# Performance work log

Hardware: AMD Instinct MI355X
Metric: run time of the kernel (lower is better)

## Reference

```python
import jax, jax.numpy as jnp
import numpy as np
from jax import lax

C = 512          # in_channels
L = 4            # fcos_conv_layers
NUM_CLS = 1      # fcos_num_class - 1
PRIOR_BIAS = float(-np.log((1 - 0.01) / 0.01))
BN_EPS = 1e-5


def conv1d(x, w, b, pad):
    # x: [B, Cin, T], w: [Cout, Cin, K]
    y = lax.conv_general_dilated(x, w, window_strides=(1,), padding=[(pad, pad)],
                                 dimension_numbers=('NCH', 'OIH', 'NCH'))
    return y + b[None, :, None]


def bn(x, g, b, m, v):
    inv = lax.rsqrt(v + BN_EPS)
    return (x - m[None, :, None]) * (g * inv)[None, :, None] + b[None, :, None]


def tower(x, ws, bs, gs, bes, ms, vs):
    # ws: [L, C, C, 3]; fixed small loop over layers
    for i in range(L):
        x = jax.nn.relu(bn(conv1d(x, ws[i], bs[i], 1), gs[i], bes[i], ms[i], vs[i]))
    return x


def setup_inputs() -> dict:
    key = jax.random.key(0)
    ks = jax.random.split(key, 32)
    d = {}
    d['f0'] = jax.random.normal(ks[0], (8, C, 1024), jnp.float32)
    d['f1'] = jax.random.normal(ks[1], (8, C, 512), jnp.float32)
    d['f2'] = jax.random.normal(ks[2], (8, C, 256), jnp.float32)

    def nrm(k, shape):
        return 0.01 * jax.random.normal(k, shape, jnp.float32)

    # cls / bbox towers: stacked conv + BN params
    d['cls_tw_w'] = nrm(ks[3], (L, C, C, 3)); d['cls_tw_b'] = jnp.zeros((L, C))
    d['cls_bn_g'] = jnp.ones((L, C)); d['cls_bn_b'] = jnp.zeros((L, C))
    d['cls_bn_m'] = jnp.zeros((L, C)); d['cls_bn_v'] = jnp.ones((L, C))
    d['box_tw_w'] = nrm(ks[4], (L, C, C, 3)); d['box_tw_b'] = jnp.zeros((L, C))
    d['box_bn_g'] = jnp.ones((L, C)); d['box_bn_b'] = jnp.zeros((L, C))
    d['box_bn_m'] = jnp.zeros((L, C)); d['box_bn_v'] = jnp.ones((L, C))

    d['logits_w'] = nrm(ks[5], (NUM_CLS, C, 3))
    d['logits_b'] = jnp.full((NUM_CLS,), PRIOR_BIAS, jnp.float32)
    d['bbox_w'] = nrm(ks[6], (2, C, 3)); d['bbox_b'] = jnp.zeros((2,))

    d['mix_w'] = nrm(ks[7], (C, 2 * C, 1)); d['mix_b'] = jnp.zeros((C,))
    d['mix_bn_g'] = jnp.ones((C,)); d['mix_bn_b'] = jnp.zeros((C,))
    d['mix_bn_m'] = jnp.zeros((C,)); d['mix_bn_v'] = jnp.ones((C,))

    d['iou_w1'] = nrm(ks[8], (C // 2, C, 3)); d['iou_b1'] = jnp.zeros((C // 2,))
    d['iou_bn_g'] = jnp.ones((C // 2,)); d['iou_bn_b'] = jnp.zeros((C // 2,))
    d['iou_bn_m'] = jnp.zeros((C // 2,)); d['iou_bn_v'] = jnp.ones((C // 2,))
    d['iou_w2'] = nrm(ks[9], (1, C // 2, 1)); d['iou_b2'] = jnp.zeros((1,))

    d['scales'] = jnp.ones((3,), jnp.float32)
    return d


def reference(f0, f1, f2,
              cls_tw_w, cls_tw_b, cls_bn_g, cls_bn_b, cls_bn_m, cls_bn_v,
              box_tw_w, box_tw_b, box_bn_g, box_bn_b, box_bn_m, box_bn_v,
              logits_w, logits_b, bbox_w, bbox_b,
              mix_w, mix_b, mix_bn_g, mix_bn_b, mix_bn_m, mix_bn_v,
              iou_w1, iou_b1, iou_bn_g, iou_bn_b, iou_bn_m, iou_bn_v,
              iou_w2, iou_b2, scales):
    outs = []
    for l, x in enumerate([f0, f1, f2]):
        ct = tower(x, cls_tw_w, cls_tw_b, cls_bn_g, cls_bn_b, cls_bn_m, cls_bn_v)
        bt = tower(x, box_tw_w, box_tw_b, box_bn_g, box_bn_b, box_bn_m, box_bn_v)
        logits = conv1d(ct, logits_w, logits_b, 1)                      # [B, 1, T]
        bbox = jnp.exp(conv1d(bt, bbox_w, bbox_b, 1) * scales[l])       # [B, 2, T]
        mix = jax.nn.relu(bn(conv1d(jnp.concatenate([ct, bt], axis=1), mix_w, mix_b, 0),
                             mix_bn_g, mix_bn_b, mix_bn_m, mix_bn_v))   # [B, C, T]
        h = jax.nn.relu(bn(conv1d(mix, iou_w1, iou_b1, 1),
                           iou_bn_g, iou_bn_b, iou_bn_m, iou_bn_v))
        iou = conv1d(h, iou_w2, iou_b2, 0)                              # [B, 1, T]
        outs.append(jnp.concatenate([logits, bbox, iou], axis=1))       # [B, 4, T]
    return jnp.concatenate(outs, axis=-1)  # [B, 4, T0+T1+T2]
```

## Files before the change

kernel.cpp:

```cpp
#include <hip/hip_runtime.h>
#include <hip/hip_bf16.h>


typedef __bf16 bf16x8 __attribute__((ext_vector_type(8)));
typedef float f32x4 __attribute__((ext_vector_type(4)));

__device__ __forceinline__ float bf2f(unsigned short u) {
    union { unsigned int i; float f; } c; c.i = ((unsigned int)u) << 16; return c.f;
}
__device__ __forceinline__ unsigned short f2bf(float f) {
    union { __hip_bfloat16 h; unsigned short u; } c; c.h = __float2bfloat16(f); return c.u;
}

__device__ __forceinline__ void gload16(const void* g, void* l) {
    __builtin_amdgcn_global_load_lds(
        (const __attribute__((address_space(1))) unsigned int*)g,
        (__attribute__((address_space(3))) unsigned int*)l,
        16, 0, 0);
}

__global__ __launch_bounds__(512, 2)
void conv_tower(const unsigned short* __restrict__ X, int xstride, int ci_twstride,
                const unsigned short* __restrict__ W,
                const float* __restrict__ Bs,
                unsigned short* __restrict__ Y)
{
    constexpr int XHALF = 17 * 512;
    constexpr int WHALF = 48 * 512;
    __shared__ alignas(16) unsigned short Xs[2 * XHALF];
    __shared__ alignas(16) unsigned short Wsh[2 * WHALF];

    const int L = blockIdx.x;
    const int P = (L & 7) * 28 + (L >> 3);
    const int tt = P >> 2, sub = P & 3;
    const int tw = sub >> 1, co0 = (sub & 1) << 8;

    int rowstart;
    if (tt < 32)      { rowstart = (tt >> 2) * 1026 + 1 + ((tt & 3) << 8); }
    else if (tt < 48) { int i = tt - 32; rowstart = 8208 + (i >> 1) * 514 + 1 + ((i & 1) << 8); }
    else              { rowstart = 12320 + (tt - 48) * 258 + 1; }

    const int tid = threadIdx.x;
    const int lane = tid & 63, wid = tid >> 6;
    const int wco = (wid >> 2) << 7;
    const int wt  = (wid & 3) << 6;
    const int lr = lane & 15;
    const int sr = lane >> 4;

    const unsigned short* Wp = W + (size_t)tw * 3145728;
    const float* Bp = Bs + tw * 2048;
    const int co_out0 = tw * 512 + co0;
    const int ci_off = tw * ci_twstride;

    const unsigned short* xga[3]; unsigned short* xl0[3];
#pragma unroll
    for (int p = 0; p < 3; ++p) {
        int seg = (p < 2) ? (p * 8 + wid) : 16;
        xl0[p] = Xs + seg * 512;
        int g = seg * 64 + lane;
        int row = g >> 2, sc = (g & 3) ^ ((row >> 1) & 3);
        xga[p] = X + (size_t)(rowstart - 1 + row) * xstride + ci_off + sc * 8;
    }
    const unsigned short* wga[6]; unsigned short* wl0[6];
#pragma unroll
    for (int p = 0; p < 6; ++p) {
        int seg = p * 8 + wid;
        wl0[p] = Wsh + seg * 512;
        int g = seg * 64 + lane;
        int row = g >> 2, sc = (g & 3) ^ ((row >> 1) & 3);
        int co = row & 255, kk = row >> 8;
        wga[p] = Wp + (size_t)(co0 + co) * 1536 + kk * 512 + sc * 8;
    }

    f32x4 acc[8][4];
#pragma unroll
    for (int i = 0; i < 8; ++i)
#pragma unroll
        for (int j = 0; j < 4; ++j) acc[i][j] = (f32x4){0.f, 0.f, 0.f, 0.f};

#pragma unroll
    for (int p = 0; p < 3; ++p) { gload16(xga[p], xl0[p]); xga[p] += 32; }
#pragma unroll
    for (int p = 0; p < 6; ++p) { gload16(wga[p], wl0[p]); wga[p] += 32; }
    asm volatile("s_waitcnt vmcnt(0)" ::: "memory");
    __builtin_amdgcn_s_barrier();

    int cur = 0;
    for (int ks = 0; ks < 16; ++ks) {
        const bool notlast = (ks < 15);
        const char* bX = (const char*)Xs + cur * (XHALF * 2);
        const char* bW = (const char*)Wsh + cur * (WHALF * 2);
#pragma unroll
        for (int kk = 0; kk < 3; ++kk) {
            bf16x8 af[8], bv[4];
#pragma unroll
            for (int mi = 0; mi < 8; ++mi) {
                int ra = kk * 256 + wco + mi * 16 + lr;
                af[mi] = *(const bf16x8*)(bW + ra * 64 + (((sr ^ (ra >> 1)) & 3) << 4));
            }
#pragma unroll
            for (int ni = 0; ni < 4; ++ni) {
                int rb = wt + ni * 16 + lr + kk;
                bv[ni] = *(const bf16x8*)(bX + rb * 64 + (((sr ^ (rb >> 1)) & 3) << 4));
            }
            if (notlast) {
                if (kk == 0) {
#pragma unroll
                    for (int p = 0; p < 3; ++p) { gload16(xga[p], xl0[p] + (cur ^ 1) * XHALF); xga[p] += 32; }
                } else {
#pragma unroll
                    for (int p = 0; p < 3; ++p) {
                        int q = (kk - 1) * 3 + p;
                        gload16(wga[q], wl0[q] + (cur ^ 1) * WHALF); wga[q] += 32;
                    }
                }
            }
            __builtin_amdgcn_s_barrier();
            asm volatile("s_waitcnt lgkmcnt(0)" ::: "memory");
            __builtin_amdgcn_sched_barrier(0);
            __builtin_amdgcn_s_setprio(1);
#pragma unroll
            for (int mi = 0; mi < 8; ++mi)
#pragma unroll
                for (int ni = 0; ni < 4; ++ni)
                    acc[mi][ni] = __builtin_amdgcn_mfma_f32_16x16x32_bf16(af[mi], bv[ni], acc[mi][ni], 0, 0, 0);
            __builtin_amdgcn_s_setprio(0);
        }
        if (notlast) asm volatile("s_waitcnt vmcnt(0)" ::: "memory");
        __builtin_amdgcn_s_barrier();
        cur ^= 1;
    }

    const int r4 = sr * 4;
#pragma unroll
    for (int mi = 0; mi < 8; ++mi) {
        int co_l = wco + mi * 16 + r4;
        float b0 = Bp[co0 + co_l + 0], b1 = Bp[co0 + co_l + 1];
        float b2 = Bp[co0 + co_l + 2], b3 = Bp[co0 + co_l + 3];
#pragma unroll
        for (int ni = 0; ni < 4; ++ni) {
            int t = wt + ni * 16 + lr;
            f32x4 a = acc[mi][ni];
            float v0 = fmaxf(a[0] + b0, 0.f), v1 = fmaxf(a[1] + b1, 0.f);
            float v2 = fmaxf(a[2] + b2, 0.f), v3 = fmaxf(a[3] + b3, 0.f);
            union { unsigned long long u; unsigned short s[4]; } pk;
            pk.s[0] = f2bf(v0); pk.s[1] = f2bf(v1); pk.s[2] = f2bf(v2); pk.s[3] = f2bf(v3);
            *(unsigned long long*)(Y + (size_t)(rowstart + t) * 1024 + co_out0 + co_l) = pk.u;
        }
    }
}

__device__ __forceinline__ void tile_decode(int ct, int& rowstart, int& t0, int& Tl) {
    if (ct < 64)      { Tl = 1024; int b = ct >> 3;                 t0 = (ct & 7) << 7; rowstart = b * 1026 + 1; }
    else if (ct < 96) { Tl = 512;  int i = ct - 64; int b = i >> 2; t0 = (i & 3) << 7; rowstart = 8208 + b * 514 + 1; }
    else              { Tl = 256;  int i = ct - 96; int b = i >> 1; t0 = (i & 1) << 7; rowstart = 12320 + b * 258 + 1; }
}

template<int KSIZE>
__global__ __launch_bounds__(256)
void conv_gemm(const unsigned short* __restrict__ X, int xstride, int ci0_base, int ci_twstride, int Cin,
               const unsigned short* __restrict__ W, int w_twstride,
               const float* __restrict__ Bs, int b_twstride,
               unsigned short* __restrict__ Y, int ystride, int co_twstride,
               int relu)
{
    constexpr int BM = 128, BN = 128, BK = 32;
    constexpr int NR = BN + KSIZE - 1;
    constexpr int XSEG = (NR * 64 + 1023) / 1024;
    constexpr int XPW  = (XSEG + 3) / 4;
    constexpr int WSEG = KSIZE * BM * 64 / 1024;
    constexpr int WPW  = WSEG / 4;
    __shared__ alignas(16) unsigned short Xs[2 * XSEG * 512];
    __shared__ alignas(16) unsigned short Ws[2 * WSEG * 512];

    const int tid = threadIdx.x;
    const int lane = tid & 63, wid = tid >> 6;
    int rowstart, t0, Tl;
    tile_decode(blockIdx.x, rowstart, t0, Tl);
    const int co0 = blockIdx.y * BM;
    const int tw = blockIdx.z;
    const int ci_off = ci0_base + tw * ci_twstride;
    const unsigned short* Wp = W + (size_t)tw * w_twstride;
    const float* Bp = Bs + tw * b_twstride;
    const int co_out0 = tw * co_twstride + co0;

    const int wm = (wid >> 1) * 64, wn = (wid & 1) * 64;
    const int lr = lane & 15;
    const int sr = lane >> 4;

    const unsigned short* xga[XPW]; unsigned short* xl[XPW];
#pragma unroll
    for (int p = 0; p < XPW; ++p) {
        int seg = (KSIZE == 3) ? ((p < 2) ? p * 4 + wid : 8) : (p * 4 + wid);
        xl[p] = Xs + seg * 512;
        int g = seg * 64 + lane;
        int row = g >> 2, s = (g & 3) ^ ((row >> 1) & 3);
        xga[p] = X + (size_t)(rowstart - (KSIZE >> 1) + row) * xstride + ci_off + s * 8;
    }
    const unsigned short* wga[WPW]; unsigned short* wl[WPW];
#pragma unroll
    for (int p = 0; p < WPW; ++p) {
        int seg = p * 4 + wid;
        wl[p] = Ws + seg * 512;
        int g = seg * 64 + lane;
        int row = g >> 2, s = (g & 3) ^ ((row >> 1) & 3);
        int co = row & (BM - 1), kk = row >> 7;
        wga[p] = Wp + (size_t)(co0 + co) * (KSIZE * Cin) + kk * Cin + s * 8;
    }

    f32x4 acc[4][4];
#pragma unroll
    for (int i = 0; i < 4; ++i)
#pragma unroll
        for (int j = 0; j < 4; ++j) acc[i][j] = (f32x4){0.f, 0.f, 0.f, 0.f};

    auto STAGE = [&](int buf) {
#pragma unroll
        for (int p = 0; p < XPW; ++p) { gload16(xga[p], xl[p] + buf * (XSEG * 512)); xga[p] += BK; }
#pragma unroll
        for (int p = 0; p < WPW; ++p) { gload16(wga[p], wl[p] + buf * (WSEG * 512)); wga[p] += BK; }
    };

    const int nk = Cin / BK;
    STAGE(0);
    int cur = 0;
    for (int ks = 0; ks < nk; ++ks) {
        if (ks + 1 < nk) {
            STAGE(cur ^ 1);
            if constexpr (KSIZE == 3) asm volatile("s_waitcnt vmcnt(9)" ::: "memory");
            else                      asm volatile("s_waitcnt vmcnt(4)" ::: "memory");
        } else {
            asm volatile("s_waitcnt vmcnt(0)" ::: "memory");
        }
        __builtin_amdgcn_sched_barrier(0);
        __builtin_amdgcn_s_barrier();

        const char* bXs = (const char*)Xs + cur * (XSEG * 1024);
        const char* bWs = (const char*)Ws + cur * (WSEG * 1024);
#pragma unroll
        for (int kk = 0; kk < KSIZE; ++kk) {
            bf16x8 af[4], bv[4];
#pragma unroll
            for (int mi = 0; mi < 4; ++mi) {
                int ra = kk * BM + wm + mi * 16 + lr;
                af[mi] = *(const bf16x8*)(bWs + ra * 64 + (((sr ^ (ra >> 1)) & 3) << 4));
                int rb = wn + mi * 16 + lr + kk;
                bv[mi] = *(const bf16x8*)(bXs + rb * 64 + (((sr ^ (rb >> 1)) & 3) << 4));
            }
#pragma unroll
            for (int mi = 0; mi < 4; ++mi)
#pragma unroll
                for (int ni = 0; ni < 4; ++ni)
                    acc[mi][ni] = __builtin_amdgcn_mfma_f32_16x16x32_bf16(af[mi], bv[ni], acc[mi][ni], 0, 0, 0);
        }
        __builtin_amdgcn_sched_barrier(0);
        __builtin_amdgcn_s_barrier();
        cur ^= 1;
    }

    const int r4 = (lane >> 4) * 4;
#pragma unroll
    for (int mi = 0; mi < 4; ++mi) {
        int co_l = wm + mi * 16 + r4;
        float b0 = Bp[co0 + co_l + 0], b1 = Bp[co0 + co_l + 1];
        float b2 = Bp[co0 + co_l + 2], b3 = Bp[co0 + co_l + 3];
#pragma unroll
        for (int ni = 0; ni < 4; ++ni) {
            int t = t0 + wn + ni * 16 + lr;
            f32x4 a = acc[mi][ni];
            float v0 = a[0] + b0, v1 = a[1] + b1, v2 = a[2] + b2, v3 = a[3] + b3;
            if (relu) {
                v0 = fmaxf(v0, 0.f); v1 = fmaxf(v1, 0.f);
                v2 = fmaxf(v2, 0.f); v3 = fmaxf(v3, 0.f);
            }
            union { unsigned long long u; unsigned short s[4]; } pk;
            pk.s[0] = f2bf(v0); pk.s[1] = f2bf(v1); pk.s[2] = f2bf(v2); pk.s[3] = f2bf(v3);
            *(unsigned long long*)(Y + (size_t)(rowstart + t) * ystride + co_out0 + co_l) = pk.u;
        }
    }
}

__global__ __launch_bounds__(256)
void zero_pads(unsigned short* __restrict__ act0, unsigned short* __restrict__ catA,
               unsigned short* __restrict__ catB, unsigned short* __restrict__ mixo,
               unsigned short* __restrict__ iouh)
{
    int c = blockIdx.x >> 1, side = blockIdx.x & 1;
    int start, Tl;
    if (c < 8)       { start = c * 1026;               Tl = 1024; }
    else if (c < 16) { start = 8208 + (c - 8) * 514;   Tl = 512;  }
    else             { start = 12320 + (c - 16) * 258; Tl = 256;  }
    size_t prow = start + (side ? Tl + 1 : 0);
    int tid = threadIdx.x;
    uint4 z = make_uint4(0u, 0u, 0u, 0u);
    if (tid < 64)  *(uint4*)(act0 + prow * 512 + tid * 8) = z;
    if (tid < 128) { *(uint4*)(catA + prow * 1024 + tid * 8) = z;
                     *(uint4*)(catB + prow * 1024 + tid * 8) = z; }
    if (tid >= 128 && tid < 192) *(uint4*)(mixo + prow * 512 + (tid - 128) * 8) = z;
    if (tid >= 192 && tid < 224) *(uint4*)(iouh + prow * 256 + (tid - 192) * 8) = z;
}

__global__ __launch_bounds__(256)
void transpose_in(const float* __restrict__ f0, const float* __restrict__ f1, const float* __restrict__ f2,
                  unsigned short* __restrict__ act0)
{
    __shared__ float tile[32][33];
    int bx = blockIdx.x;
    const float* src; int Tl, padbase, b, t0;
    if (bx < 256)      { src = f0; Tl = 1024; int i = bx;       b = i >> 5; t0 = (i & 31) << 5; padbase = b * 1026; }
    else if (bx < 384) { src = f1; Tl = 512;  int i = bx - 256; b = i >> 4; t0 = (i & 15) << 5; padbase = 8208 + b * 514; }
    else               { src = f2; Tl = 256;  int i = bx - 384; b = i >> 3; t0 = (i & 7)  << 5; padbase = 12320 + b * 258; }
    int c0 = blockIdx.y << 5;
    const float* sb = src + (size_t)b * 512 * Tl;
    int tl = threadIdx.x & 31, cl = threadIdx.x >> 5;
#pragma unroll
    for (int j = 0; j < 4; ++j) {
        int c = cl + j * 8;
        tile[c][tl] = sb[(size_t)(c0 + c) * Tl + t0 + tl];
    }
    __syncthreads();
    int cc = threadIdx.x & 31, tr0 = threadIdx.x >> 5;
    size_t base = (size_t)(padbase + 1 + t0) * 512 + c0;
#pragma unroll
    for (int j = 0; j < 4; ++j) {
        int tr = tr0 + j * 8;
        act0[base + (size_t)tr * 512 + cc] = f2bf(tile[cc][tr]);
    }
}

__global__ __launch_bounds__(256)
void prep_tower(const float* __restrict__ cls_w, const float* __restrict__ box_w,
                const float* __restrict__ cg, const float* __restrict__ cvv,
                const float* __restrict__ bg, const float* __restrict__ bvv,
                unsigned short* __restrict__ Wt)
{
    int idx = blockIdx.x * 256 + threadIdx.x;
    if (idx >= 2 * 4 * 512 * 3 * 512) return;
    int ci = idx & 511;
    int kk = (idx >> 9) % 3;
    int co = (idx / 1536) & 511;
    int l  = (idx / 786432) & 3;
    int tw = idx / 3145728;
    const float* w = tw ? box_w : cls_w;
    const float* g = tw ? bg : cg;
    const float* v = tw ? bvv : cvv;
    float s = g[l * 512 + co] * rsqrtf(v[l * 512 + co] + 1e-5f);
    float val = w[(((size_t)(l * 512 + co)) * 512 + ci) * 3 + kk] * s;
    Wt[idx] = f2bf(val);
}

__global__ __launch_bounds__(256)
void prep_misc(const float* mix_w, const float* mix_b, const float* mg, const float* mbeta, const float* mm, const float* mv,
               const float* iou_w1, const float* iou_b1, const float* ig, const float* ibeta, const float* im, const float* iv,
               const float* cls_b, const float* cg, const float* cbeta, const float* cm, const float* cv2,
               const float* box_b, const float* bg, const float* bbeta, const float* bm, const float* bv2,
               unsigned short* Wmix, unsigned short* Wiou, float* Bt, float* Bmix, float* Biou)
{
    int idx = blockIdx.x * 256 + threadIdx.x;
    if (idx < 524288) {
        int co = idx >> 10;
        float s = mg[co] * rsqrtf(mv[co] + 1e-5f);
        Wmix[idx] = f2bf(mix_w[idx] * s);
        return;
    }
    idx -= 524288;
    if (idx < 393216) {
        int ci = idx & 511, kk = (idx >> 9) % 3, co = idx / 1536;
        float s = ig[co] * rsqrtf(iv[co] + 1e-5f);
        Wiou[idx] = f2bf(iou_w1[((size_t)(co * 512 + ci)) * 3 + kk] * s);
        return;
    }
    idx -= 393216;
    if (idx < 4096) {
        int co = idx & 511, l = (idx >> 9) & 3, tw = idx >> 11;
        const float* g = tw ? bg : cg; const float* v = tw ? bv2 : cv2;
        const float* m = tw ? bm : cm; const float* be = tw ? bbeta : cbeta;
        const float* cb = tw ? box_b : cls_b;
        int o = l * 512 + co;
        float s = g[o] * rsqrtf(v[o] + 1e-5f);
        Bt[idx] = (cb[o] - m[o]) * s + be[o];
        return;
    }
    idx -= 4096;
    if (idx < 512) {
        float s = mg[idx] * rsqrtf(mv[idx] + 1e-5f);
        Bmix[idx] = (mix_b[idx] - mm[idx]) * s + mbeta[idx];
        return;
    }
    idx -= 512;
    if (idx < 256) {
        float s = ig[idx] * rsqrtf(iv[idx] + 1e-5f);
        Biou[idx] = (iou_b1[idx] - im[idx]) * s + ibeta[idx];
    }
}

__global__ __launch_bounds__(256)
void heads_kernel(const unsigned short* __restrict__ catb, const unsigned short* __restrict__ iouh,
                  const float* __restrict__ lw, const float* __restrict__ lb,
                  const float* __restrict__ bw, const float* __restrict__ bb,
                  const float* __restrict__ iw, const float* __restrict__ ib,
                  const float* __restrict__ scales, float* __restrict__ out)
{
    const int lane = threadIdx.x & 63;
    const int wid = threadIdx.x >> 6;

    float lwr[24], bwr0[24], bwr1[24], iwr[4];
    {
        const float4* p = (const float4*)(lw + lane * 24);
#pragma unroll
        for (int q = 0; q < 6; ++q) {
            float4 v = p[q];
            lwr[q * 4 + 0] = v.x; lwr[q * 4 + 1] = v.y; lwr[q * 4 + 2] = v.z; lwr[q * 4 + 3] = v.w;
        }
        p = (const float4*)(bw + lane * 24);
#pragma unroll
        for (int q = 0; q < 6; ++q) {
            float4 v = p[q];
            bwr0[q * 4 + 0] = v.x; bwr0[q * 4 + 1] = v.y; bwr0[q * 4 + 2] = v.z; bwr0[q * 4 + 3] = v.w;
        }
        p = (const float4*)(bw + 1536 + lane * 24);
#pragma unroll
        for (int q = 0; q < 6; ++q) {
            float4 v = p[q];
            bwr1[q * 4 + 0] = v.x; bwr1[q * 4 + 1] = v.y; bwr1[q * 4 + 2] = v.z; bwr1[q * 4 + 3] = v.w;
        }
        float4 v = *(const float4*)(iw + lane * 4);
        iwr[0] = v.x; iwr[1] = v.y; iwr[2] = v.z; iwr[3] = v.w;
    }
    const float lb0 = lb[0], bb0 = bb[0], bb1 = bb[1], ib0 = ib[0];
    const float s0 = scales[0], s1 = scales[1], s2 = scales[2];

    for (int r = blockIdx.x * 4 + wid; r < 14336; r += gridDim.x * 4) {
        int tlog, roff, tgoff, padbase; float sc;
        if (r < 8192)       { tlog = 10; roff = 0;     tgoff = 0;    sc = s0; }
        else if (r < 12288) { tlog = 9;  roff = 8192;  tgoff = 1024; sc = s1; }
        else                { tlog = 8;  roff = 12288; tgoff = 1536; sc = s2; }
        int i = r - roff;
        int Tl = 1 << tlog;
        int b = i >> tlog, t = i & (Tl - 1);
        if (r < 8192)       padbase = b * 1026;
        else if (r < 12288) padbase = 8208 + b * 514;
        else                padbase = 12320 + b * 258;
        int prow = padbase + 1 + t;

        float al = 0.f, a0 = 0.f, a1 = 0.f, ai = 0.f;
        const unsigned short* base = catb + (size_t)prow * 1024 + lane * 8;
#pragma unroll
        for (int kk = 0; kk < 3; ++kk) {
            union { uint4 u; unsigned short s[8]; } cv, bv;
            cv.u = *(const uint4*)(base + (kk - 1) * 1024);
            bv.u = *(const uint4*)(base + (kk - 1) * 1024 + 512);
#pragma unroll
            for (int j = 0; j < 8; ++j) {
                float xc = bf2f(cv.s[j]);
                float xb = bf2f(bv.s[j]);
                al = fmaf(xc, lwr[j * 3 + kk], al);
                a0 = fmaf(xb, bwr0[j * 3 + kk], a0);
                a1 = fmaf(xb, bwr1[j * 3 + kk], a1);
            }
        }
        {
            union { uint2 u; unsigned short s[4]; } hv;
            hv.u = *(const uint2*)(iouh + (size_t)prow * 256 + lane * 4);
#pragma unroll
            for (int j = 0; j < 4; ++j) ai = fmaf(bf2f(hv.s[j]), iwr[j], ai);
        }
#pragma unroll
        for (int off = 32; off > 0; off >>= 1) {
            al += __shfl_xor(al, off);
            a0 += __shfl_xor(a0, off);
            a1 += __shfl_xor(a1, off);
            ai += __shfl_xor(ai, off);
        }
        if (lane == 0) {
            int tg = tgoff + t;
            out[((size_t)b * 4 + 0) * 1792 + tg] = al + lb0;
            out[((size_t)b * 4 + 1) * 1792 + tg] = expf((a0 + bb0) * sc);
            out[((size_t)b * 4 + 2) * 1792 + tg] = expf((a1 + bb1) * sc);
            out[((size_t)b * 4 + 3) * 1792 + tg] = ai + ib0;
        }
    }
}

extern "C" void kernel_launch(void* const* d_in, const int* in_sizes, int n_in,
                              void* d_out, int out_size, void* d_ws, size_t ws_size,
                              hipStream_t stream)
{
    const float* f0       = (const float*)d_in[0];
    const float* f1       = (const float*)d_in[1];
    const float* f2       = (const float*)d_in[2];
    const float* cls_tw_w = (const float*)d_in[3];
    const float* cls_tw_b = (const float*)d_in[4];
    const float* cls_bn_g = (const float*)d_in[5];
    const float* cls_bn_b = (const float*)d_in[6];
    const float* cls_bn_m = (const float*)d_in[7];
    const float* cls_bn_v = (const float*)d_in[8];
    const float* box_tw_w = (const float*)d_in[9];
    const float* box_tw_b = (const float*)d_in[10];
    const float* box_bn_g = (const float*)d_in[11];
    const float* box_bn_b = (const float*)d_in[12];
    const float* box_bn_m = (const float*)d_in[13];
    const float* box_bn_v = (const float*)d_in[14];
    const float* logits_w = (const float*)d_in[15];
    const float* logits_b = (const float*)d_in[16];
    const float* bbox_w   = (const float*)d_in[17];
    const float* bbox_b   = (const float*)d_in[18];
    const float* mix_w    = (const float*)d_in[19];
    const float* mix_b    = (const float*)d_in[20];
    const float* mix_bn_g = (const float*)d_in[21];
    const float* mix_bn_b = (const float*)d_in[22];
    const float* mix_bn_m = (const float*)d_in[23];
    const float* mix_bn_v = (const float*)d_in[24];
    const float* iou_w1   = (const float*)d_in[25];
    const float* iou_b1   = (const float*)d_in[26];
    const float* iou_bn_g = (const float*)d_in[27];
    const float* iou_bn_b = (const float*)d_in[28];
    const float* iou_bn_m = (const float*)d_in[29];
    const float* iou_bn_v = (const float*)d_in[30];
    const float* iou_w2   = (const float*)d_in[31];
    const float* iou_b2   = (const float*)d_in[32];
    const float* scales   = (const float*)d_in[33];

    unsigned char* ws = (unsigned char*)d_ws;
    unsigned short* Wt   = (unsigned short*)(ws + 0);
    unsigned short* Wmix = (unsigned short*)(ws + 12582912);
    unsigned short* Wiou = (unsigned short*)(ws + 13631488);
    float*          Bt   = (float*)(ws + 14417920);
    float*          Bmix = (float*)(ws + 14434304);
    float*          Biou = (float*)(ws + 14436352);
    unsigned short* act0 = (unsigned short*)(ws + 14437376);
    unsigned short* catA = (unsigned short*)(ws + 29182976);
    unsigned short* catB = (unsigned short*)(ws + 58674176);
    unsigned short* mixo = (unsigned short*)(ws + 88165376);
    unsigned short* iouh = (unsigned short*)(ws + 102910976);

    zero_pads<<<dim3(48), dim3(256), 0, stream>>>(act0, catA, catB, mixo, iouh);
    prep_tower<<<dim3(24576), dim3(256), 0, stream>>>(cls_tw_w, box_tw_w, cls_bn_g, cls_bn_v,
                                                      box_bn_g, box_bn_v, Wt);
    prep_misc<<<dim3(3603), dim3(256), 0, stream>>>(mix_w, mix_b, mix_bn_g, mix_bn_b, mix_bn_m, mix_bn_v,
                                                    iou_w1, iou_b1, iou_bn_g, iou_bn_b, iou_bn_m, iou_bn_v,
                                                    cls_tw_b, cls_bn_g, cls_bn_b, cls_bn_m, cls_bn_v,
                                                    box_tw_b, box_bn_g, box_bn_b, box_bn_m, box_bn_v,
                                                    Wmix, Wiou, Bt, Bmix, Biou);
    transpose_in<<<dim3(448, 16), dim3(256), 0, stream>>>(f0, f1, f2, act0);

    conv_tower<<<dim3(224), dim3(512), 0, stream>>>(act0, 512, 0,   Wt,            Bt,        catA);
    conv_tower<<<dim3(224), dim3(512), 0, stream>>>(catA, 1024, 512, Wt + 786432,  Bt + 512,  catB);
    conv_tower<<<dim3(224), dim3(512), 0, stream>>>(catB, 1024, 512, Wt + 1572864, Bt + 1024, catA);
    conv_tower<<<dim3(224), dim3(512), 0, stream>>>(catA, 1024, 512, Wt + 2359296, Bt + 1536, catB);
    conv_gemm<1><<<dim3(112, 4, 1), 256, 0, stream>>>(catB, 1024, 0, 0, 1024,
                                                      Wmix, 0, Bmix, 0, mixo, 512, 0, 1);
    conv_gemm<3><<<dim3(112, 2, 1), 256, 0, stream>>>(mixo, 512, 0, 0, 512,
                                                      Wiou, 0, Biou, 0, iouh, 256, 0, 1);
    heads_kernel<<<dim3(896), dim3(256), 0, stream>>>(catB, iouh, logits_w, logits_b,
                                                      bbox_w, bbox_b, iou_w2, iou_b2, scales,
                                                      (float*)d_out);
}
```

Before: 293.1 us.

## Restructure conv tower GEMM into per-tap pipeline with register double-buffered fragments

Changes the conv_tower main loop from 16 k-steps with three taps each into a flat 48-stage pipeline. Weights now use a triple-buffered per-tap LDS ring and X a double buffer, and the next stage's A/B fragments are prefetched into registers before the current MFMAs. LDS offsets are precomputed. The aim is to hide LDS read latency behind MFMA work and shrink weight LDS from two 48-row halves to three 16-row buffers. In exchange it raises register pressure, fully unrolls 48 stages (code size), and adds a vmcnt wait plus a barrier at every stage.

```diff
diff --git a/kernel.cpp b/kernel.cpp
--- a/kernel.cpp
+++ b/kernel.cpp
@@ -25,10 +25,8 @@
                 const float* __restrict__ Bs,
                 unsigned short* __restrict__ Y)
 {
-    constexpr int XHALF = 17 * 512;
-    constexpr int WHALF = 48 * 512;
-    __shared__ alignas(16) unsigned short Xs[2 * XHALF];
-    __shared__ alignas(16) unsigned short Wsh[2 * WHALF];
+    __shared__ alignas(16) unsigned short Xb[2][17 * 512];
+    __shared__ alignas(16) unsigned short Wb[3][16 * 512];
 
     const int L = blockIdx.x;
     const int P = (L & 7) * 28 + (L >> 3);
@@ -52,25 +50,41 @@
     const int co_out0 = tw * 512 + co0;
     const int ci_off = tw * ci_twstride;
 
-    const unsigned short* xga[3]; unsigned short* xl0[3];
+    const unsigned short* xga[3]; unsigned short* xl[3];
 #pragma unroll
     for (int p = 0; p < 3; ++p) {
         int seg = (p < 2) ? (p * 8 + wid) : 16;
-        xl0[p] = Xs + seg * 512;
+        xl[p] = (unsigned short*)Xb[0] + seg * 512;
         int g = seg * 64 + lane;
         int row = g >> 2, sc = (g & 3) ^ ((row >> 1) & 3);
         xga[p] = X + (size_t)(rowstart - 1 + row) * xstride + ci_off + sc * 8;
     }
-    const unsigned short* wga[6]; unsigned short* wl0[6];
-#pragma unroll
-    for (int p = 0; p < 6; ++p) {
+    const unsigned short* wga[2]; unsigned short* wl[2];
+#pragma unroll
+    for (int p = 0; p < 2; ++p) {
         int seg = p * 8 + wid;
-        wl0[p] = Wsh + seg * 512;
+        wl[p] = (unsigned short*)Wb[0] + seg * 512;
         int g = seg * 64 + lane;
         int row = g >> 2, sc = (g & 3) ^ ((row >> 1) & 3);
-        int co = row & 255, kk = row >> 8;
-        wga[p] = Wp + (size_t)(co0 + co) * 1536 + kk * 512 + sc * 8;
-    }
+        wga[p] = Wp + (size_t)(co0 + row) * 1536 + sc * 8;
+    }
+    constexpr int XBSZ = 17 * 512;
+    constexpr int WBSZ = 16 * 512;
+
+    int aoff[8];
+#pragma unroll
+    for (int mi = 0; mi < 8; ++mi) {
+        int ra = wco + mi * 16 + lr;
+        aoff[mi] = ra * 64 + (((sr ^ (ra >> 1)) & 3) << 4);
+    }
+    int boff[3][4];
+#pragma unroll
+    for (int kk = 0; kk < 3; ++kk)
+#pragma unroll
+        for (int ni = 0; ni < 4; ++ni) {
+            int rb = wt + ni * 16 + lr + kk;
+            boff[kk][ni] = rb * 64 + (((sr ^ (rb >> 1)) & 3) << 4);
+        }
 
     f32x4 acc[8][4];
 #pragma unroll
@@ -79,56 +93,57 @@
         for (int j = 0; j < 4; ++j) acc[i][j] = (f32x4){0.f, 0.f, 0.f, 0.f};
 
 #pragma unroll
-    for (int p = 0; p < 3; ++p) { gload16(xga[p], xl0[p]); xga[p] += 32; }
-#pragma unroll
-    for (int p = 0; p < 6; ++p) { gload16(wga[p], wl0[p]); wga[p] += 32; }
+    for (int p = 0; p < 3; ++p) gload16(xga[p], xl[p]);
+#pragma unroll
+    for (int p = 0; p < 2; ++p) {
+        gload16(wga[p],       wl[p]);
+        gload16(wga[p] + 512, wl[p] + WBSZ);
+    }
     asm volatile("s_waitcnt vmcnt(0)" ::: "memory");
     __builtin_amdgcn_s_barrier();
 
-    int cur = 0;
-    for (int ks = 0; ks < 16; ++ks) {
-        const bool notlast = (ks < 15);
-        const char* bX = (const char*)Xs + cur * (XHALF * 2);
-        const char* bW = (const char*)Wsh + cur * (WHALF * 2);
-#pragma unroll
-        for (int kk = 0; kk < 3; ++kk) {
-            bf16x8 af[8], bv[4];
-#pragma unroll
-            for (int mi = 0; mi < 8; ++mi) {
-                int ra = kk * 256 + wco + mi * 16 + lr;
-                af[mi] = *(const bf16x8*)(bW + ra * 64 + (((sr ^ (ra >> 1)) & 3) << 4));
-            }
-#pragma unroll
-            for (int ni = 0; ni < 4; ++ni) {
-                int rb = wt + ni * 16 + lr + kk;
-                bv[ni] = *(const bf16x8*)(bX + rb * 64 + (((sr ^ (rb >> 1)) & 3) << 4));
-            }
-            if (notlast) {
-                if (kk == 0) {
-#pragma unroll
-                    for (int p = 0; p < 3; ++p) { gload16(xga[p], xl0[p] + (cur ^ 1) * XHALF); xga[p] += 32; }
-                } else {
-#pragma unroll
-                    for (int p = 0; p < 3; ++p) {
-                        int q = (kk - 1) * 3 + p;
-                        gload16(wga[q], wl0[q] + (cur ^ 1) * WHALF); wga[q] += 32;
-                    }
-                }
-            }
-            __builtin_amdgcn_s_barrier();
-            asm volatile("s_waitcnt lgkmcnt(0)" ::: "memory");
-            __builtin_amdgcn_sched_barrier(0);
-            __builtin_amdgcn_s_setprio(1);
+    bf16x8 af[2][8], bv[2][4];
+#pragma unroll
+    for (int mi = 0; mi < 8; ++mi) af[0][mi] = *(const bf16x8*)((const char*)Wb[0] + aoff[mi]);
+#pragma unroll
+    for (int ni = 0; ni < 4; ++ni) bv[0][ni] = *(const bf16x8*)((const char*)Xb[0] + boff[0][ni]);
+
+#pragma unroll
+    for (int s = 0; s < 48; ++s) {
+        const int cr = s & 1, nx = cr ^ 1;
+        const int ks = s / 3;
+        if (s < 46) {
+            const int sp = s + 2;
+            const int tap2 = sp % 3, ks2 = sp / 3;
+#pragma unroll
+            for (int p = 0; p < 2; ++p)
+                gload16(wga[p] + tap2 * 512 + ks2 * 32, wl[p] + (sp % 3) * WBSZ);
+        }
+        if ((s % 3) == 0 && ks < 15) {
+#pragma unroll
+            for (int p = 0; p < 3; ++p)
+                gload16(xga[p] + (ks + 1) * 32, xl[p] + ((ks + 1) & 1) * XBSZ);
+        }
+        if (s < 47) {
+            const int sn = s + 1;
+            const int tapn = sn % 3, wbn = sn % 3, xbn = (sn / 3) & 1;
 #pragma unroll
             for (int mi = 0; mi < 8; ++mi)
-#pragma unroll
-                for (int ni = 0; ni < 4; ++ni)
-                    acc[mi][ni] = __builtin_amdgcn_mfma_f32_16x16x32_bf16(af[mi], bv[ni], acc[mi][ni], 0, 0, 0);
-            __builtin_amdgcn_s_setprio(0);
-        }
-        if (notlast) asm volatile("s_waitcnt vmcnt(0)" ::: "memory");
+                af[nx][mi] = *(const bf16x8*)((const char*)Wb[wbn] + aoff[mi]);
+#pragma unroll
+            for (int ni = 0; ni < 4; ++ni)
+                bv[nx][ni] = *(const bf16x8*)((const char*)Xb[xbn] + boff[tapn][ni]);
+        }
+        __builtin_amdgcn_sched_barrier(0);
+        __builtin_amdgcn_s_setprio(1);
+#pragma unroll
+        for (int mi = 0; mi < 8; ++mi)
+#pragma unroll
+            for (int ni = 0; ni < 4; ++ni)
+                acc[mi][ni] = __builtin_amdgcn_mfma_f32_16x16x32_bf16(af[cr][mi], bv[cr][ni], acc[mi][ni], 0, 0, 0);
+        __builtin_amdgcn_s_setprio(0);
+        asm volatile("s_waitcnt vmcnt(0)" ::: "memory");
         __builtin_amdgcn_s_barrier();
-        cur ^= 1;
     }
 
     const int r4 = sr * 4;
@@ -447,13 +462,13 @@
         const unsigned short* base = catb + (size_t)prow * 1024 + lane * 8;
 #pragma unroll
         for (int kk = 0; kk < 3; ++kk) {
-            union { uint4 u; unsigned short s[8]; } cv, bv;
+            union { uint4 u; unsigned short s[8]; } cv, bvv;
             cv.u = *(const uint4*)(base + (kk - 1) * 1024);
-            bv.u = *(const uint4*)(base + (kk - 1) * 1024 + 512);
+            bvv.u = *(const uint4*)(base + (kk - 1) * 1024 + 512);
 #pragma unroll
             for (int j = 0; j < 8; ++j) {
                 float xc = bf2f(cv.s[j]);
-                float xb = bf2f(bv.s[j]);
+                float xb = bf2f(bvv.s[j]);
                 al = fmaf(xc, lwr[j * 3 + kk], al);
                 a0 = fmaf(xb, bwr0[j * 3 + kk], a0);
                 a1 = fmaf(xb, bwr1[j * 3 + kk], a1);
```

Measured after the change: 298.3 us. Within noise of the previous version (+1.8%).
